# Optimization experiments

Hardware: AMD Instinct MI355X
Metric: run time of the kernel (lower is better)

## Reference

```python
import jax, jax.numpy as jnp
import numpy as np

C = 256
CK = C // 8  # query/key projection dim

def conv1x1(x, w, b):
    # x: (B,C,H,W), w: (O,C), b: (O,)
    return jnp.einsum('bchw,oc->bohw', x, w) + b[None, :, None, None]

def conv3x3(x, w, b):
    # w: (O,C,3,3)
    y = jax.lax.conv_general_dilated(x, w, window_strides=(1, 1), padding='SAME',
                                     dimension_numbers=('NCHW', 'OIHW', 'NCHW'))
    return y + b[None, :, None, None]

def setup_inputs() -> dict:
    key = jax.random.key(0)
    ks = jax.random.split(key, 24)
    s = 0.05
    d = {
        'x1': jax.random.normal(ks[0], (4, C, 64, 64), jnp.float32),
        'x2': jax.random.normal(ks[1], (4, C, 64, 64), jnp.float32),
        'wq1': jax.random.normal(ks[2], (CK, C), jnp.float32) * s,
        'bq1': jax.random.normal(ks[3], (CK,), jnp.float32) * s,
        'wk1': jax.random.normal(ks[4], (CK, C), jnp.float32) * s,
        'bk1': jax.random.normal(ks[5], (CK,), jnp.float32) * s,
        'wv1': jax.random.normal(ks[6], (C, C), jnp.float32) * s,
        'bv1': jax.random.normal(ks[7], (C,), jnp.float32) * s,
        'wq2': jax.random.normal(ks[8], (CK, C), jnp.float32) * s,
        'bq2': jax.random.normal(ks[9], (CK,), jnp.float32) * s,
        'wk2': jax.random.normal(ks[10], (CK, C), jnp.float32) * s,
        'bk2': jax.random.normal(ks[11], (CK,), jnp.float32) * s,
        'wv2': jax.random.normal(ks[12], (C, C), jnp.float32) * s,
        'bv2': jax.random.normal(ks[13], (C,), jnp.float32) * s,
        'wd1': jax.random.normal(ks[14], (C, C), jnp.float32) * s,
        'bd1': jax.random.normal(ks[15], (C,), jnp.float32) * s,
        'wd3': jax.random.normal(ks[16], (C, C, 3, 3), jnp.float32) * s,
        'bd3': jax.random.normal(ks[17], (C,), jnp.float32) * s,
        'gamma1': jax.random.normal(ks[18], (1,), jnp.float32) * 0.5,
        'gamma2': jax.random.normal(ks[19], (1,), jnp.float32) * 0.5,
    }
    return d

def reference(x1, x2, wq1, bq1, wk1, bk1, wv1, bv1, wq2, bq2, wk2, bk2, wv2, bv2,
              wd1, bd1, wd3, bd3, gamma1, gamma2):
    B, Cc, H, W = x1.shape
    N = H * W
    # projections (1x1 convs), flattened to (B, d, N)
    q1 = conv1x1(x1, wq1, bq1).reshape(B, CK, N)
    k1 = conv1x1(x1, wk1, bk1).reshape(B, CK, N)
    v1 = conv1x1(x1, wv1, bv1).reshape(B, Cc, N)
    q2 = conv1x1(x2, wq2, bq2).reshape(B, CK, N)
    k2 = conv1x1(x2, wk2, bk2).reshape(B, CK, N)
    v2 = conv1x1(x2, wv2, bv2).reshape(B, Cc, N)
    # cross attention 1: queries from x1, keys/values from x2
    energy1 = jnp.einsum('bdi,bdj->bij', q1, k2)          # (B,N,N)
    attn1 = jax.nn.softmax(energy1, axis=-1)
    out1 = jnp.einsum('bcj,bij->bci', v2, attn1).reshape(B, Cc, H, W)
    # cross attention 2: queries from x2, keys/values from x1
    energy2 = jnp.einsum('bdi,bdj->bij', q2, k1)
    attn2 = jax.nn.softmax(energy2, axis=-1)
    out2 = jnp.einsum('bcj,bij->bci', v1, attn2).reshape(B, Cc, H, W)
    # residual conv branches + gamma-scaled skip (norm1/norm2 in source are dead code)
    out1 = out1 + conv1x1(x1, wd1, bd1) + conv3x3(x1, wd3, bd3)
    out2 = out2 + conv1x1(x2, wd1, bd1) + conv3x3(x2, wd3, bd3)
    out1 = x1 + gamma1[0] * out1
    out2 = x2 + gamma2[0] * out2
    return (out1, out2)
```

## Files before the change

kernel.cpp:

```cpp
#include <hip/hip_runtime.h>
#include <hip/hip_bf16.h>

#define CC 256
#define CKD 32
#define NN 4096
#define HH 64
#define WW 64
#define BB 4

#define LOG2E 1.44269504088896f
#define EXPSHIFT 23.0831203874f

typedef __attribute__((ext_vector_type(8))) short short8;
typedef __attribute__((ext_vector_type(4))) float floatx4;

__device__ __forceinline__ unsigned f2bf(float f) {
  union { float f; unsigned u; } v; v.f = f;
  unsigned r = v.u + 0x7fffu + ((v.u >> 16) & 1u);
  return r >> 16;
}
__device__ __forceinline__ unsigned f2bf_fast(float f) {
  return (__float_as_uint(f) + 0x8000u) >> 16;
}
__device__ __forceinline__ float fast_exp2(float x) {
#if __has_builtin(__builtin_amdgcn_exp2f)
  return __builtin_amdgcn_exp2f(x);
#else
  return __expf(x * 0.693147181f);
#endif
}
__device__ __forceinline__ float bf_lo(unsigned u) { return __uint_as_float(u << 16); }
__device__ __forceinline__ float bf_hi(unsigned u) { return __uint_as_float(u & 0xffff0000u); }

__global__ __launch_bounds__(256) void xpack_kernel(
    const float* __restrict__ x1, const float* __restrict__ x2,
    unsigned short* __restrict__ Xp) {
  const int t = threadIdx.x;
  const int nb = blockIdx.x, cbk = blockIdx.y, img = blockIdx.z;
  const float* X = ((img >> 2) ? x2 : x1) + (size_t)(img & 3) * CC * NN;
  const int n0 = nb * 64, c0 = cbk * 64;
  __shared__ float tile[64][65];
  const int nl = t & 63, cl0 = t >> 6;
#pragma unroll
  for (int i = 0; i < 16; ++i)
    tile[cl0 + i * 4][nl] = X[(size_t)(c0 + cl0 + i * 4) * NN + n0 + nl];
  __syncthreads();
#pragma unroll
  for (int it = 0; it < 2; ++it) {
    int id = it * 256 + t;
    int nl2 = id >> 3, cc = id & 7;
    short8 v;
#pragma unroll
    for (int j = 0; j < 8; ++j) v[j] = (short)f2bf(tile[cc * 8 + j][nl2]);
    *(short8*)(Xp + (size_t)img * NN * CC + (size_t)(n0 + nl2) * CC + c0 + cc * 8) = v;
  }
}

__global__ __launch_bounds__(256) void wpack_kernel(
    const float* __restrict__ wd1, const float* __restrict__ wd3,
    const float* __restrict__ wq1, const float* __restrict__ wk1,
    const float* __restrict__ wv1,
    const float* __restrict__ wq2, const float* __restrict__ wk2,
    const float* __restrict__ wv2,
    const float* __restrict__ bq1, const float* __restrict__ bk1,
    const float* __restrict__ bv1,
    const float* __restrict__ bq2, const float* __restrict__ bk2,
    const float* __restrict__ bv2,
    unsigned short* __restrict__ Wp, unsigned short* __restrict__ Wqkv,
    float* __restrict__ Bias) {
  const int id = blockIdx.x * 256 + threadIdx.x;
#pragma unroll
  for (int tap = 0; tap < 10; ++tap) {
    float v = (tap < 9) ? wd3[(size_t)id * 9 + tap] : wd1[id];
    Wp[(size_t)tap * (CC * CC) + id] = (unsigned short)f2bf(v);
  }
#pragma unroll
  for (int j = 0; j < 3; ++j) {
    int e = id + j * 65536;
    if (e < 2 * 320 * 256) {
      int inp = e / (320 * 256), rem = e % (320 * 256);
      int o = rem >> 8, c = rem & 255;
      float v;
      if (inp == 0)
        v = (o < 32) ? wq1[o * 256 + c] * LOG2E
            : (o < 64) ? wk1[(o - 32) * 256 + c] : wv1[(o - 64) * 256 + c];
      else
        v = (o < 32) ? wq2[o * 256 + c] * LOG2E
            : (o < 64) ? wk2[(o - 32) * 256 + c] : wv2[(o - 64) * 256 + c];
      Wqkv[e] = (unsigned short)f2bf(v);
    }
  }
  if (id < 640) {
    int inp = id / 320, o = id % 320;
    float v;
    if (inp == 0) v = (o < 32) ? bq1[o] * LOG2E
                      : (o < 64) ? bk1[o - 32] : bv1[o - 64];
    else          v = (o < 32) ? bq2[o] * LOG2E
                      : (o < 64) ? bk2[o - 32] : bv2[o - 64];
    Bias[id] = v;
  }
}

__global__ __launch_bounds__(256) void proj_mfma_kernel(
    const unsigned short* __restrict__ Xp, const unsigned short* __restrict__ Wqkv,
    const float* __restrict__ Bias,
    unsigned short* __restrict__ Qp1, unsigned short* __restrict__ Kp1,
    unsigned short* __restrict__ Vp1,
    unsigned short* __restrict__ Qp2, unsigned short* __restrict__ Kp2,
    unsigned short* __restrict__ Vp2) {
  const int t = threadIdx.x;
  const int w = t >> 6, lane = t & 63;
  const int l15 = lane & 15, g = lane >> 4;
  const int img = blockIdx.x, pb = blockIdx.y;
  const int pix0 = pb * 64;
  const int inp = img >> 2, b = img & 3;
  const unsigned short* Xi = Xp + (size_t)img * NN * CC;
  const unsigned short* Wb = Wqkv + (size_t)inp * 320 * CC;
  const float* Bi = Bias + inp * 320;
  unsigned short* Qp = (inp ? Qp2 : Qp1) + (size_t)b * NN * CKD;
  unsigned short* Kp = (inp ? Kp2 : Kp1) + (size_t)b * NN * CKD;
  unsigned short* Vp = (inp ? Vp2 : Vp1) + (size_t)b * NN * CC;

  __shared__ unsigned short tile[320][72];

  floatx4 acc[4][5];
#pragma unroll
  for (int mf = 0; mf < 4; ++mf)
#pragma unroll
    for (int nf = 0; nf < 5; ++nf) acc[mf][nf] = (floatx4){0.f, 0.f, 0.f, 0.f};
  const int o0w = w * 80;

#pragma unroll
  for (int cb = 0; cb < 8; ++cb) {
    short8 a[4], bfr[5];
#pragma unroll
    for (int mf = 0; mf < 4; ++mf)
      a[mf] = *(const short8*)(Xi + (size_t)(pix0 + mf * 16 + l15) * CC + cb * 32 + g * 8);
#pragma unroll
    for (int nf = 0; nf < 5; ++nf)
      bfr[nf] = *(const short8*)(Wb + (size_t)(o0w + nf * 16 + l15) * CC + cb * 32 + g * 8);
#pragma unroll
    for (int nf = 0; nf < 5; ++nf)
#pragma unroll
      for (int mf = 0; mf < 4; ++mf)
        acc[mf][nf] = __builtin_amdgcn_mfma_f32_16x16x32_bf16(
            a[mf], bfr[nf], acc[mf][nf], 0, 0, 0);
  }

#pragma unroll
  for (int nf = 0; nf < 5; ++nf) {
    float bs = Bi[o0w + nf * 16 + l15];
#pragma unroll
    for (int mf = 0; mf < 4; ++mf) {
      uint2 pk;
      pk.x = f2bf(acc[mf][nf][0] + bs) | (f2bf(acc[mf][nf][1] + bs) << 16);
      pk.y = f2bf(acc[mf][nf][2] + bs) | (f2bf(acc[mf][nf][3] + bs) << 16);
      *(uint2*)&tile[o0w + nf * 16 + l15][mf * 16 + g * 4] = pk;
    }
  }
  __syncthreads();

  {
    const int pix = t >> 2, ch = t & 3;
    short8 vq, vk;
#pragma unroll
    for (int e = 0; e < 8; ++e) {
      vq[e] = (short)tile[ch * 8 + e][pix];
      vk[e] = (short)tile[32 + ch * 8 + e][pix];
    }
    *(short8*)(Qp + (size_t)(pix0 + pix) * CKD + ch * 8) = vq;
    *(short8*)(Kp + (size_t)(pix0 + pix) * CKD + ch * 8) = vk;
  }
#pragma unroll
  for (int it = 0; it < 8; ++it) {
    short8 vv = *(const short8*)&tile[64 + t][it * 8];
    *(short8*)(Vp + ((size_t)((pix0 >> 3) + it) * CC + t) * 8) = vv;
  }
}

__global__ __launch_bounds__(256, 2) void attn_kernel(
    const unsigned short* __restrict__ Qp1, const unsigned short* __restrict__ Kp1,
    const unsigned short* __restrict__ Qp2, const unsigned short* __restrict__ Kp2,
    const unsigned short* __restrict__ Vp1, const unsigned short* __restrict__ Vp2,
    const unsigned short* __restrict__ Xp, const unsigned short* __restrict__ Wp,
    const float* __restrict__ bd1, const float* __restrict__ bd3,
    const float* __restrict__ x1, const float* __restrict__ x2,
    const float* __restrict__ g1, const float* __restrict__ g2,
    float* __restrict__ out) {
  const int t = threadIdx.x;
  const int w = t >> 6, lane = t & 63;
  const int l15 = lane & 15, g = lane >> 4;
  const int att = blockIdx.x, b = blockIdx.y;
  const int yblk = blockIdx.z;
  const int i0 = yblk * 64;

  const unsigned short *Qp, *Kp, *Vp; const float *x; float gamma; float* o;
  if (att == 0) { Qp = Qp1; Kp = Kp2; Vp = Vp2; x = x1; gamma = g1[0]; o = out; }
  else          { Qp = Qp2; Kp = Kp1; Vp = Vp1; x = x2; gamma = g2[0];
                  o = out + (size_t)BB * CC * NN; }
  Qp += (size_t)b * NN * CKD; Kp += (size_t)b * NN * CKD; Vp += (size_t)b * NN * CC;
  x += (size_t)b * CC * NN; o += (size_t)b * CC * NN;
  const unsigned short* Xi = Xp + (size_t)(att * 4 + b) * NN * CC;

  __shared__ union {
    unsigned short xs[3][66][72];
    unsigned short ps[2][64][72];
  } u;
  __shared__ unsigned short cres[256][68];
  __shared__ float l_s[64];

  short8 bq = *(const short8*)(Qp + (size_t)(i0 + w * 16 + l15) * CKD + g * 8);

  floatx4 acc[4][4];
#pragma unroll
  for (int a = 0; a < 4; ++a)
#pragma unroll
    for (int c = 0; c < 4; ++c) acc[a][c] = (floatx4){0.f, 0.f, 0.f, 0.f};
  float l_acc = 0.f;
  const floatx4 zinit = {-EXPSHIFT, -EXPSHIFT, -EXPSHIFT, -EXPSHIFT};

  short8 kr[2][4], vr[2][8];
  auto LOADK = [&](int tt, short8* d) {
    const unsigned short* kb = Kp + ((size_t)tt * 64 + l15) * CKD + g * 8;
#pragma unroll
    for (int js = 0; js < 4; ++js) d[js] = *(const short8*)(kb + js * 16 * CKD);
  };
  auto LOADV = [&](int tt, short8* d) {
#pragma unroll
    for (int ks = 0; ks < 2; ++ks)
#pragma unroll
      for (int cs = 0; cs < 4; ++cs)
        d[ks * 4 + cs] = *(const short8*)(Vp +
            (((size_t)tt * 8 + ks * 4 + g) * CC + (w * 64 + cs * 16 + l15)) * 8);
  };
  auto GEMM1 = [&](const short8* kb, unsigned short (*ps)[72]) {
#pragma unroll
    for (int js = 0; js < 4; ++js) {
      floatx4 s = __builtin_amdgcn_mfma_f32_16x16x32_bf16(kb[js], bq, zinit, 0, 0, 0);
      float p0 = fast_exp2(s[0]);
      float p1 = fast_exp2(s[1]);
      float p2 = fast_exp2(s[2]);
      float p3 = fast_exp2(s[3]);
      l_acc += (p0 + p1) + (p2 + p3);
      unsigned u0 = __float_as_uint(p0) + 0x8000u;
      unsigned u1 = __float_as_uint(p1) + 0x8000u;
      unsigned u2 = __float_as_uint(p2) + 0x8000u;
      unsigned u3 = __float_as_uint(p3) + 0x8000u;
      uint2 pk;
      pk.x = __builtin_amdgcn_perm(u1, u0, 0x07060302u);
      pk.y = __builtin_amdgcn_perm(u3, u2, 0x07060302u);
      *(uint2*)&ps[w * 16 + l15][js * 16 + g * 4] = pk;
    }
  };
  auto GEMM2 = [&](const short8* vb, unsigned short (*ps)[72]) {
#pragma unroll
    for (int ks = 0; ks < 2; ++ks) {
      short8 ap[4];
#pragma unroll
      for (int isub = 0; isub < 4; ++isub)
        ap[isub] = *(const short8*)&ps[isub * 16 + l15][ks * 32 + g * 8];
#pragma unroll
      for (int cs = 0; cs < 4; ++cs)
#pragma unroll
        for (int isub = 0; isub < 4; ++isub)
          acc[isub][cs] = __builtin_amdgcn_mfma_f32_16x16x32_bf16(
              ap[isub], vb[ks * 4 + cs], acc[isub][cs], 0, 0, 0);
    }
  };

  LOADK(0, kr[0]); LOADK(1, kr[1]); LOADV(0, vr[0]);

  {
    floatx4 ac[4][4];
#pragma unroll
    for (int pm = 0; pm < 4; ++pm)
#pragma unroll
      for (int on = 0; on < 4; ++on) ac[pm][on] = (floatx4){0.f, 0.f, 0.f, 0.f};

    for (int cb = 0; cb < 4; ++cb) {
      const int c0 = cb * 64;
      if (cb) __syncthreads();
#pragma unroll
      for (int it = 0; it < 7; ++it) {
        int id = it * 256 + t;
        if (id < 1584) {
          int r = id / 528, rem = id % 528;
          int col = rem >> 3, cc = rem & 7;
          int y = yblk - 1 + r, xx = col - 1;
          short8 v = {0, 0, 0, 0, 0, 0, 0, 0};
          if (y >= 0 && y < HH && xx >= 0 && xx < WW)
            v = *(const short8*)(Xi + (size_t)(y * WW + xx) * CC + c0 + cc * 8);
          *(short8*)&u.xs[r][col][cc * 8] = v;
        }
      }
      __syncthreads();
#pragma unroll
      for (int tap = 0; tap < 10; ++tap) {
        const int dy = (tap < 9) ? tap / 3 - 1 : 0;
        const int dx = (tap < 9) ? tap % 3 - 1 : 0;
        const unsigned short* wrow =
            Wp + ((size_t)tap * CC + w * 64 + l15) * CC + c0 + g * 8;
#pragma unroll
        for (int ks = 0; ks < 2; ++ks) {
          short8 af[4], bw[4];
#pragma unroll
          for (int pm = 0; pm < 4; ++pm)
            af[pm] = *(const short8*)&u.xs[1 + dy][1 + pm * 16 + l15 + dx][ks * 32 + g * 8];
#pragma unroll
          for (int on = 0; on < 4; ++on)
            bw[on] = *(const short8*)(wrow + (size_t)(on * 16) * CC + ks * 32);
#pragma unroll
          for (int pm = 0; pm < 4; ++pm)
#pragma unroll
            for (int on = 0; on < 4; ++on)
              ac[pm][on] = __builtin_amdgcn_mfma_f32_16x16x32_bf16(
                  af[pm], bw[on], ac[pm][on], 0, 0, 0);
        }
      }
    }
#pragma unroll
    for (int on = 0; on < 4; ++on) {
      int oo = w * 64 + on * 16 + l15;
      float bs = bd1[oo] + bd3[oo];
#pragma unroll
      for (int pm = 0; pm < 4; ++pm) {
        uint2 pk;
        pk.x = f2bf_fast(ac[pm][on][0] + bs) | (f2bf_fast(ac[pm][on][1] + bs) << 16);
        pk.y = f2bf_fast(ac[pm][on][2] + bs) | (f2bf_fast(ac[pm][on][3] + bs) << 16);
        *(uint2*)&cres[oo][pm * 16 + g * 4] = pk;
      }
    }
  }
  __syncthreads();

  GEMM1(kr[0], u.ps[0]);
  __syncthreads();

  for (int jt = 0; jt < 64; jt += 2) {
    if (jt + 2 < 64) LOADK(jt + 2, kr[0]);
    LOADV(jt + 1, vr[1]);
    GEMM1(kr[1], u.ps[1]);
    GEMM2(vr[0], u.ps[0]);
    __syncthreads();
    if (jt + 3 < 64) LOADK(jt + 3, kr[1]);
    if (jt + 2 < 64) { LOADV(jt + 2, vr[0]); GEMM1(kr[0], u.ps[0]); }
    GEMM2(vr[1], u.ps[1]);
    __syncthreads();
  }

  l_acc += __shfl_xor(l_acc, 16);
  l_acc += __shfl_xor(l_acc, 32);
  if (g == 0) l_s[w * 16 + l15] = l_acc;
  __syncthreads();

#pragma unroll
  for (int isub = 0; isub < 4; ++isub) {
    float linv[4];
#pragma unroll
    for (int r = 0; r < 4; ++r) linv[r] = 1.f / l_s[isub * 16 + g * 4 + r];
#pragma unroll
    for (int cs = 0; cs < 4; ++cs) {
      int c = w * 64 + cs * 16 + l15;
      size_t base = (size_t)c * NN + i0 + isub * 16 + g * 4;
      float4 xr = *(const float4*)(x + base);
      uint2 cr = *(const uint2*)&cres[c][isub * 16 + g * 4];
      float4 ov;
      ov.x = xr.x + gamma * (acc[isub][cs][0] * linv[0] + bf_lo(cr.x));
      ov.y = xr.y + gamma * (acc[isub][cs][1] * linv[1] + bf_hi(cr.x));
      ov.z = xr.z + gamma * (acc[isub][cs][2] * linv[2] + bf_lo(cr.y));
      ov.w = xr.w + gamma * (acc[isub][cs][3] * linv[3] + bf_hi(cr.y));
      *(float4*)(o + base) = ov;
    }
  }
}

extern "C" void kernel_launch(void* const* d_in, const int* in_sizes, int n_in,
                              void* d_out, int out_size, void* d_ws, size_t ws_size,
                              hipStream_t stream) {
  const float* x1  = (const float*)d_in[0];
  const float* x2  = (const float*)d_in[1];
  const float* wq1 = (const float*)d_in[2];
  const float* bq1 = (const float*)d_in[3];
  const float* wk1 = (const float*)d_in[4];
  const float* bk1 = (const float*)d_in[5];
  const float* wv1 = (const float*)d_in[6];
  const float* bv1 = (const float*)d_in[7];
  const float* wq2 = (const float*)d_in[8];
  const float* bq2 = (const float*)d_in[9];
  const float* wk2 = (const float*)d_in[10];
  const float* bk2 = (const float*)d_in[11];
  const float* wv2 = (const float*)d_in[12];
  const float* bv2 = (const float*)d_in[13];
  const float* wd1 = (const float*)d_in[14];
  const float* bd1 = (const float*)d_in[15];
  const float* wd3 = (const float*)d_in[16];
  const float* bd3 = (const float*)d_in[17];
  const float* g1  = (const float*)d_in[18];
  const float* g2  = (const float*)d_in[19];
  float* out = (float*)d_out;

  const size_t QB = (size_t)BB * NN * CKD * 2;
  const size_t VB = (size_t)BB * NN * CC * 2;
  const size_t XB = (size_t)2 * BB * NN * CC * 2;
  const size_t WPB = (size_t)10 * CC * CC * 2;
  const size_t WQB = (size_t)2 * 320 * CC * 2;
  char* base = (char*)d_ws;
  unsigned short* Qp1 = (unsigned short*)(base);
  unsigned short* Kp1 = (unsigned short*)(base + QB);
  unsigned short* Qp2 = (unsigned short*)(base + 2 * QB);
  unsigned short* Kp2 = (unsigned short*)(base + 3 * QB);
  unsigned short* Vp1 = (unsigned short*)(base + 4 * QB);
  unsigned short* Vp2 = (unsigned short*)(base + 4 * QB + VB);
  unsigned short* Xp  = (unsigned short*)(base + 4 * QB + 2 * VB);
  unsigned short* Wp  = (unsigned short*)(base + 4 * QB + 2 * VB + XB);
  unsigned short* Wqkv = (unsigned short*)(base + 4 * QB + 2 * VB + XB + WPB);
  float* Bias = (float*)(base + 4 * QB + 2 * VB + XB + WPB + WQB);

  xpack_kernel<<<dim3(NN / 64, CC / 64, 2 * BB), 256, 0, stream>>>(x1, x2, Xp);
  wpack_kernel<<<dim3(CC * CC / 256), 256, 0, stream>>>(
      wd1, wd3, wq1, wk1, wv1, wq2, wk2, wv2,
      bq1, bk1, bv1, bq2, bk2, bv2, Wp, Wqkv, Bias);

  proj_mfma_kernel<<<dim3(2 * BB, NN / 64), 256, 0, stream>>>(
      Xp, Wqkv, Bias, Qp1, Kp1, Vp1, Qp2, Kp2, Vp2);

  attn_kernel<<<dim3(2, BB, NN / 64), 256, 0, stream>>>(
      Qp1, Kp1, Qp2, Kp2, Vp1, Vp2, Xp, Wp, bd1, bd3, x1, x2, g1, g2, out);
}
```

Measured before the change: 303.9 us.

## Keep attention probabilities in registers and drop LDS staging and barriers

Each wave now computes the score tile for all 64 queries itself, so the probabilities come out of the first MFMA already in the register layout the PV MFMA needs. This removes the shared-memory P buffer and the per-tile __syncthreads. The V packing kernel permutes its channel ordering to match that layout, and the PV MFMAs are wrapped in s_setprio. The cost is that QK^T and exp work is duplicated across the four waves, and the prefetch loads tiles 64 and 65 past the end of the key and value data.

```diff
diff --git a/kernel.cpp b/kernel.cpp
--- a/kernel.cpp
+++ b/kernel.cpp
@@ -31,6 +31,11 @@
 }
 __device__ __forceinline__ float bf_lo(unsigned u) { return __uint_as_float(u << 16); }
 __device__ __forceinline__ float bf_hi(unsigned u) { return __uint_as_float(u & 0xffff0000u); }
+__device__ __forceinline__ unsigned pack2bf(float a, float b) {
+  unsigned ua = __float_as_uint(a) + 0x8000u;
+  unsigned ub = __float_as_uint(b) + 0x8000u;
+  return __builtin_amdgcn_perm(ub, ua, 0x07060302u);
+}
 
 __global__ __launch_bounds__(256) void xpack_kernel(
     const float* __restrict__ x1, const float* __restrict__ x2,
@@ -172,9 +177,12 @@
     *(short8*)(Kp + (size_t)(pix0 + pix) * CKD + ch * 8) = vk;
   }
 #pragma unroll
-  for (int it = 0; it < 8; ++it) {
-    short8 vv = *(const short8*)&tile[64 + t][it * 8];
-    *(short8*)(Vp + ((size_t)((pix0 >> 3) + it) * CC + t) * 8) = vv;
+  for (int gi = 0; gi < 8; ++gi) {
+    const int h = gi >> 2, gg = gi & 3;
+    uint2 lo = *(const uint2*)&tile[64 + t][h * 32 + gg * 4];
+    uint2 hi = *(const uint2*)&tile[64 + t][h * 32 + 16 + gg * 4];
+    uint4 vv = {lo.x, lo.y, hi.x, hi.y};
+    *(uint4*)(Vp + (((size_t)(pix0 >> 3) + gi) * CC + t) * 8) = vv;
   }
 }
 
@@ -202,73 +210,65 @@
   x += (size_t)b * CC * NN; o += (size_t)b * CC * NN;
   const unsigned short* Xi = Xp + (size_t)(att * 4 + b) * NN * CC;
 
-  __shared__ union {
-    unsigned short xs[3][66][72];
-    unsigned short ps[2][64][72];
-  } u;
+  __shared__ unsigned short xs[3][66][72];
   __shared__ unsigned short cres[256][68];
   __shared__ float l_s[64];
 
-  short8 bq = *(const short8*)(Qp + (size_t)(i0 + w * 16 + l15) * CKD + g * 8);
+  short8 bq[4];
+#pragma unroll
+  for (int iq = 0; iq < 4; ++iq)
+    bq[iq] = *(const short8*)(Qp + (size_t)(i0 + iq * 16 + l15) * CKD + g * 8);
 
   floatx4 acc[4][4];
 #pragma unroll
   for (int a = 0; a < 4; ++a)
 #pragma unroll
     for (int c = 0; c < 4; ++c) acc[a][c] = (floatx4){0.f, 0.f, 0.f, 0.f};
-  float l_acc = 0.f;
+  float l_acc[4] = {0.f, 0.f, 0.f, 0.f};
   const floatx4 zinit = {-EXPSHIFT, -EXPSHIFT, -EXPSHIFT, -EXPSHIFT};
 
-  short8 kr[2][4], vr[2][8];
+  short8 kr0[4], kr1[4], vr0[4], vr1[4], paA[4], paB[4];
   auto LOADK = [&](int tt, short8* d) {
     const unsigned short* kb = Kp + ((size_t)tt * 64 + l15) * CKD + g * 8;
 #pragma unroll
     for (int js = 0; js < 4; ++js) d[js] = *(const short8*)(kb + js * 16 * CKD);
   };
-  auto LOADV = [&](int tt, short8* d) {
-#pragma unroll
-    for (int ks = 0; ks < 2; ++ks)
-#pragma unroll
-      for (int cs = 0; cs < 4; ++cs)
-        d[ks * 4 + cs] = *(const short8*)(Vp +
-            (((size_t)tt * 8 + ks * 4 + g) * CC + (w * 64 + cs * 16 + l15)) * 8);
+  auto LOADVH = [&](int tt, int h, short8* d) {
+#pragma unroll
+    for (int cs = 0; cs < 4; ++cs)
+      d[cs] = *(const short8*)(Vp +
+          (((size_t)tt * 8 + h * 4 + g) * CC + (w * 64 + cs * 16 + l15)) * 8);
   };
-  auto GEMM1 = [&](const short8* kb, unsigned short (*ps)[72]) {
-#pragma unroll
-    for (int js = 0; js < 4; ++js) {
-      floatx4 s = __builtin_amdgcn_mfma_f32_16x16x32_bf16(kb[js], bq, zinit, 0, 0, 0);
-      float p0 = fast_exp2(s[0]);
-      float p1 = fast_exp2(s[1]);
-      float p2 = fast_exp2(s[2]);
-      float p3 = fast_exp2(s[3]);
-      l_acc += (p0 + p1) + (p2 + p3);
-      unsigned u0 = __float_as_uint(p0) + 0x8000u;
-      unsigned u1 = __float_as_uint(p1) + 0x8000u;
-      unsigned u2 = __float_as_uint(p2) + 0x8000u;
-      unsigned u3 = __float_as_uint(p3) + 0x8000u;
-      uint2 pk;
-      pk.x = __builtin_amdgcn_perm(u1, u0, 0x07060302u);
-      pk.y = __builtin_amdgcn_perm(u3, u2, 0x07060302u);
-      *(uint2*)&ps[w * 16 + l15][js * 16 + g * 4] = pk;
+  auto G1H = [&](const short8& kbA, const short8& kbB, short8* pa) {
+#pragma unroll
+    for (int iq = 0; iq < 4; ++iq) {
+      floatx4 s0 = __builtin_amdgcn_mfma_f32_16x16x32_bf16(kbA, bq[iq], zinit, 0, 0, 0);
+      floatx4 s1 = __builtin_amdgcn_mfma_f32_16x16x32_bf16(kbB, bq[iq], zinit, 0, 0, 0);
+      float p0 = fast_exp2(s0[0]), p1 = fast_exp2(s0[1]);
+      float p2 = fast_exp2(s0[2]), p3 = fast_exp2(s0[3]);
+      float p4 = fast_exp2(s1[0]), p5 = fast_exp2(s1[1]);
+      float p6 = fast_exp2(s1[2]), p7 = fast_exp2(s1[3]);
+      l_acc[iq] += ((p0 + p1) + (p2 + p3)) + ((p4 + p5) + (p6 + p7));
+      union { unsigned u[4]; short8 s; } cv;
+      cv.u[0] = pack2bf(p0, p1);
+      cv.u[1] = pack2bf(p2, p3);
+      cv.u[2] = pack2bf(p4, p5);
+      cv.u[3] = pack2bf(p6, p7);
+      pa[iq] = cv.s;
     }
   };
-  auto GEMM2 = [&](const short8* vb, unsigned short (*ps)[72]) {
-#pragma unroll
-    for (int ks = 0; ks < 2; ++ks) {
-      short8 ap[4];
+  auto G2H = [&](const short8* pa, const short8* vb) {
+    __builtin_amdgcn_s_setprio(1);
+#pragma unroll
+    for (int cs = 0; cs < 4; ++cs)
 #pragma unroll
       for (int isub = 0; isub < 4; ++isub)
-        ap[isub] = *(const short8*)&ps[isub * 16 + l15][ks * 32 + g * 8];
-#pragma unroll
-      for (int cs = 0; cs < 4; ++cs)
-#pragma unroll
-        for (int isub = 0; isub < 4; ++isub)
-          acc[isub][cs] = __builtin_amdgcn_mfma_f32_16x16x32_bf16(
-              ap[isub], vb[ks * 4 + cs], acc[isub][cs], 0, 0, 0);
-    }
+        acc[isub][cs] = __builtin_amdgcn_mfma_f32_16x16x32_bf16(
+            pa[isub], vb[cs], acc[isub][cs], 0, 0, 0);
+    __builtin_amdgcn_s_setprio(0);
   };
 
-  LOADK(0, kr[0]); LOADK(1, kr[1]); LOADV(0, vr[0]);
+  LOADK(0, kr0); LOADK(1, kr1); LOADVH(0, 0, vr0); LOADVH(0, 1, vr1);
 
   {
     floatx4 ac[4][4];
@@ -290,7 +290,7 @@
           short8 v = {0, 0, 0, 0, 0, 0, 0, 0};
           if (y >= 0 && y < HH && xx >= 0 && xx < WW)
             v = *(const short8*)(Xi + (size_t)(y * WW + xx) * CC + c0 + cc * 8);
-          *(short8*)&u.xs[r][col][cc * 8] = v;
+          *(short8*)&xs[r][col][cc * 8] = v;
         }
       }
       __syncthreads();
@@ -305,7 +305,7 @@
           short8 af[4], bw[4];
 #pragma unroll
           for (int pm = 0; pm < 4; ++pm)
-            af[pm] = *(const short8*)&u.xs[1 + dy][1 + pm * 16 + l15 + dx][ks * 32 + g * 8];
+            af[pm] = *(const short8*)&xs[1 + dy][1 + pm * 16 + l15 + dx][ks * 32 + g * 8];
 #pragma unroll
           for (int on = 0; on < 4; ++on)
             bw[on] = *(const short8*)(wrow + (size_t)(on * 16) * CC + ks * 32);
@@ -331,26 +331,31 @@
       }
     }
   }
-  __syncthreads();
-
-  GEMM1(kr[0], u.ps[0]);
-  __syncthreads();
 
   for (int jt = 0; jt < 64; jt += 2) {
-    if (jt + 2 < 64) LOADK(jt + 2, kr[0]);
-    LOADV(jt + 1, vr[1]);
-    GEMM1(kr[1], u.ps[1]);
-    GEMM2(vr[0], u.ps[0]);
-    __syncthreads();
-    if (jt + 3 < 64) LOADK(jt + 3, kr[1]);
-    if (jt + 2 < 64) { LOADV(jt + 2, vr[0]); GEMM1(kr[0], u.ps[0]); }
-    GEMM2(vr[1], u.ps[1]);
-    __syncthreads();
-  }
-
-  l_acc += __shfl_xor(l_acc, 16);
-  l_acc += __shfl_xor(l_acc, 32);
-  if (g == 0) l_s[w * 16 + l15] = l_acc;
+    G1H(kr0[0], kr0[1], paA);
+    G2H(paA, vr0);
+    LOADVH(jt + 1, 0, vr0);
+    G1H(kr0[2], kr0[3], paB);
+    LOADK(jt + 2, kr0);
+    G2H(paB, vr1);
+    LOADVH(jt + 1, 1, vr1);
+    G1H(kr1[0], kr1[1], paA);
+    G2H(paA, vr0);
+    LOADVH(jt + 2, 0, vr0);
+    G1H(kr1[2], kr1[3], paB);
+    LOADK(jt + 3, kr1);
+    G2H(paB, vr1);
+    LOADVH(jt + 2, 1, vr1);
+  }
+
+#pragma unroll
+  for (int iq = 0; iq < 4; ++iq) {
+    float v = l_acc[iq];
+    v += __shfl_xor(v, 16);
+    v += __shfl_xor(v, 32);
+    if (w == 0 && g == 0) l_s[iq * 16 + l15] = v;
+  }
   __syncthreads();
 
 #pragma unroll
```

Measured after the change: 486.4 us. 1.6x slower.
